# Optimization experiments

Measured on AMD Instinct MI355X. Metric: run time of the kernel, lower is better.

## Reference

```python
import jax, jax.numpy as jnp
from jax import lax
import numpy as np

T, B, D = 1024, 2, 1024
E, TOP_K, ED, HD, MAXP = 12, 4, 256, 64, 64
H = ED // HD  # num_heads = 4


def setup_inputs() -> dict:
    rng = jax.random.key(0)
    ks = jax.random.split(rng, 9)
    s = 0.02
    return {
        "query": jax.random.normal(ks[0], (T, B, D), jnp.float32),
        "key": jax.random.normal(ks[1], (T, B, D), jnp.float32),
        "value": jax.random.normal(ks[2], (T, B, D), jnp.float32),
        "w_gate": jax.random.normal(ks[3], (D, E), jnp.float32) * s,
        "w_map": jax.random.normal(ks[4], (E, D, ED), jnp.float32) * s,
        "w_reduce": jax.random.normal(ks[5], (E, ED, D), jnp.float32) * s,
        "wk": jax.random.normal(ks[6], (D, ED), jnp.float32) * s,
        "wv": jax.random.normal(ks[7], (D, ED), jnp.float32) * s,
        "rel_pos_emb": jax.random.normal(ks[8], (H, HD, 2 * MAXP + 1), jnp.float32) * s,
    }


def reference(query, key, value, w_gate, w_map, w_reduce, wk, wv, rel_pos_emb):
    t, b, d = query.shape
    n = t * b
    scaling = HD ** (-0.25)

    # ---- MoE map (q projection): softmax gating, top-k dispatch ----
    x = query.reshape(n, d)
    probs = jax.nn.softmax(x @ w_gate, axis=-1)          # [N,E]
    gates, idx = lax.top_k(probs, TOP_K)                 # [N,K]
    all_map = jnp.einsum('nd,edh->neh', x, w_map)        # [N,E,ED]
    q = jnp.take_along_axis(all_map, idx[:, :, None], axis=1)  # [N,K,ED]

    # ---- dense k/v projections ----
    q = (q * scaling).reshape(t, b, TOP_K, H, HD).transpose(1, 2, 3, 0, 4)  # [B,K,H,T,HD]
    k = (key.reshape(n, d) @ wk * scaling).reshape(t, b, H, HD).transpose(1, 2, 0, 3)  # [B,H,S,HD]
    v = (value.reshape(n, d) @ wv).reshape(t, b, H, HD).transpose(1, 2, 0, 3)          # [B,H,S,HD]

    # ---- attention scores ----
    aw = jnp.einsum('bkhie,bhje->bkhij', q, k)           # [B,K,H,T,S]

    # ---- relative position logits (einsum + gather) ----
    s_len = t
    pos = jnp.arange(s_len)
    grid = jnp.clip(pos[None, :] - pos[:, None], 1 - MAXP, MAXP - 1) + MAXP  # [T,S]
    rel = jnp.einsum('bkhid,hdp->bkhip', q, rel_pos_emb)  # [B,K,H,T,2*MAXP+1]
    rel_g = rel[:, :, :, jnp.arange(t)[:, None], grid]    # [B,K,H,T,S]

    aw = jax.nn.softmax(aw + rel_g, axis=-1)
    attn = jnp.einsum('bkhij,bhje->bkhie', aw, v)         # [B,K,H,T,HD]

    # ---- MoE reduce (combine with gates) ----
    a = attn.transpose(3, 0, 1, 2, 4).reshape(n, TOP_K, ED)  # [N,K,ED]
    one_hot = jax.nn.one_hot(idx, E, dtype=a.dtype)          # [N,K,E]
    z = jnp.einsum('nkh,nke,nk->neh', a, one_hot, gates)     # [N,E,ED]
    out = jnp.einsum('neh,ehd->nd', z, w_reduce)             # [N,D]
    return out.reshape(t, b, d)
```

## Files before the change

kernel.cpp:

```cpp
#include <hip/hip_runtime.h>

#define T_    1024
#define B_    2
#define D_    1024
#define E_    12
#define TOPK  4
#define ED_   256
#define HD_   64
#define H_    4
#define N_    (T_*B_)
#define NROW  (N_*TOPK)
#define PB3_MAX 76
#define KA_   256

typedef __bf16 bf16x8 __attribute__((ext_vector_type(8)));
typedef _Float16 f16x8 __attribute__((ext_vector_type(8)));
typedef float  f32x4  __attribute__((ext_vector_type(4)));

__device__ __forceinline__ float sc_() { return 0.35355339059327373f; }

__device__ __forceinline__ void async16(const void* g, void* l) {
    __builtin_amdgcn_global_load_lds((const __attribute__((address_space(1))) void*)g,
                                     (__attribute__((address_space(3))) void*)l, 16, 0, 0);
}

#define PREP_GRID 8324
__global__ void __launch_bounds__(256)
prep_kernel(const float* __restrict__ query, const float* __restrict__ key,
            const float* __restrict__ value, const float* __restrict__ wg,
            const float* __restrict__ wmap, const float* __restrict__ wred,
            const float* __restrict__ wk, const float* __restrict__ wv,
            const float* __restrict__ rpe,
            float* __restrict__ gates, int* __restrict__ idx, ushort* __restrict__ xb,
            ushort* __restrict__ keyb, ushort* __restrict__ valb,
            ushort* __restrict__ wmapT, ushort* __restrict__ wredf,
            ushort* __restrict__ wkT, ushort* __restrict__ wvT,
            ushort* __restrict__ rpeT, float* __restrict__ out) {
    __shared__ __align__(16) float lsbuf[12288];
    int bid = blockIdx.x, tid = threadIdx.x;

    if (bid < 512) {
        float (*lsw)[1024] = (float(*)[1024])lsbuf;
        for (int i = tid; i < 12288; i += 256) {
            int d = i / 12, e = i - d * 12;
            lsw[e][d] = wg[i];
        }
        __syncthreads();
        int w = tid >> 6, L = tid & 63;
        int n = bid * 4 + w;
        const float* xr = query + (size_t)n * D_;
        float acc[E_];
#pragma unroll
        for (int e = 0; e < E_; ++e) acc[e] = 0.f;
#pragma unroll
        for (int it = 0; it < 4; ++it) {
            float4 xv = *(const float4*)(xr + it * 256 + L * 4);
            union { __bf16 h[4]; uint2 u; } pk;
            pk.h[0] = (__bf16)xv.x; pk.h[1] = (__bf16)xv.y;
            pk.h[2] = (__bf16)xv.z; pk.h[3] = (__bf16)xv.w;
            *(uint2*)(xb + (size_t)n * D_ + it * 256 + L * 4) = pk.u;
#pragma unroll
            for (int e = 0; e < E_; ++e) {
                float4 wvv = *(const float4*)(&lsw[e][it * 256 + L * 4]);
                acc[e] += xv.x * wvv.x + xv.y * wvv.y + xv.z * wvv.z + xv.w * wvv.w;
            }
        }
#pragma unroll
        for (int e = 0; e < E_; ++e) {
            float v = acc[e];
            for (int o = 32; o > 0; o >>= 1) v += __shfl_down(v, o);
            acc[e] = v;
        }
        if (L == 0) {
            float mx = acc[0];
            for (int e = 1; e < E_; ++e) mx = fmaxf(mx, acc[e]);
            float s = 0.f, pr[E_];
            for (int e = 0; e < E_; ++e) { pr[e] = expf(acc[e] - mx); s += pr[e]; }
            float inv = 1.f / s;
            for (int e = 0; e < E_; ++e) pr[e] *= inv;
            for (int k = 0; k < TOPK; ++k) {
                int be = 0; float bv = -1.f;
                for (int e = 0; e < E_; ++e) if (pr[e] > bv) { bv = pr[e]; be = e; }
                gates[n * TOPK + k] = bv;
                idx[n * TOPK + k] = be;
                pr[be] = -1.f;
            }
        }
    } else if (bid < 1280) {
        float (*ls)[65] = (float(*)[65])lsbuf;
        int i = bid - 512;
        int e = i >> 6, rem = i & 63, et = rem >> 4, dt = rem & 15;
        int c = tid & 63, rg = tid >> 6;
        const float* src = wred + (size_t)e * (ED_ * D_) + (size_t)(et * 64) * D_ + dt * 64;
#pragma unroll
        for (int q = 0; q < 16; ++q) {
            int r = q * 4 + rg;
            ls[r][c] = src[(size_t)r * D_ + c];
        }
        __syncthreads();
        ushort* dst = wredf + (size_t)e * (D_ * KA_) + (size_t)(dt * 64) * KA_ + et * 64;
#pragma unroll
        for (int q = 0; q < 16; ++q) {
            int r = q * 4 + rg;
            union { _Float16 h; ushort u; } cv; cv.h = (_Float16)ls[c][r];
            dst[(size_t)r * KA_ + c] = cv.u;
        }
    } else if (bid < 5376) {
        int g = (bid - 1280) * 256 + tid;
        int which = g >> 19, t = g & ((1 << 19) - 1);
        const float* src = which ? value : key;
        ushort* dst = which ? valb : keyb;
        float4 v = *(const float4*)(src + (size_t)t * 4);
        union { __bf16 h[4]; uint2 u; } pk;
        pk.h[0] = (__bf16)v.x; pk.h[1] = (__bf16)v.y;
        pk.h[2] = (__bf16)v.z; pk.h[3] = (__bf16)v.w;
        *(uint2*)(dst + (size_t)t * 4) = pk.u;
    } else if (bid < 6144) {
        float (*ls)[65] = (float(*)[65])lsbuf;
        int i = bid - 5376;
        int e = i >> 6, rem = i & 63, dt = rem >> 2, et = rem & 3;
        int c = tid & 63, rg = tid >> 6;
        const float* src = wmap + (size_t)e * (D_ * ED_) + (size_t)(dt * 64) * ED_ + et * 64;
#pragma unroll
        for (int q = 0; q < 16; ++q) {
            int r = q * 4 + rg;
            ls[r][c] = src[(size_t)r * ED_ + c];
        }
        __syncthreads();
        ushort* dst = wmapT + ((size_t)e << 18) + (size_t)(et * 64) * 1024 + dt * 64;
#pragma unroll
        for (int q = 0; q < 16; ++q) {
            int r = q * 4 + rg;
            union { __bf16 h; ushort u; } cv; cv.h = (__bf16)ls[c][r];
            dst[(size_t)r * 1024 + c] = cv.u;
        }
    } else if (bid < 8192) {
        int t = (bid - 6144) * 256 + tid;
        *(float4*)(out + (size_t)t * 4) = make_float4(0.f, 0.f, 0.f, 0.f);
    } else if (bid < 8320) {
        float (*ls)[65] = (float(*)[65])lsbuf;
        int i = bid - 8192;
        int which = i >> 6, rem = i & 63, dt = rem >> 2, et = rem & 3;
        const float* w = which ? wv : wk;
        ushort* wT = which ? wvT : wkT;
        int c = tid & 63, rg = tid >> 6;
        const float* src = w + (size_t)(dt * 64) * ED_ + et * 64;
#pragma unroll
        for (int q = 0; q < 16; ++q) {
            int r = q * 4 + rg;
            ls[r][c] = src[(size_t)r * ED_ + c];
        }
        __syncthreads();
        ushort* dst = wT + (size_t)(et * 64) * 1024 + dt * 64;
#pragma unroll
        for (int q = 0; q < 16; ++q) {
            int r = q * 4 + rg;
            union { __bf16 h; ushort u; } cv; cv.h = (__bf16)ls[c][r];
            dst[(size_t)r * 1024 + c] = cv.u;
        }
    } else {
        int h = bid - 8320;
        int p = tid & 127, dq = tid >> 7;
#pragma unroll
        for (int d0 = 0; d0 < 64; d0 += 2) {
            int d = d0 + dq;
            union { __bf16 b; ushort u; } cv;
            cv.b = (__bf16)rpe[(size_t)(h * 64 + d) * 129 + p];
            rpeT[(size_t)(h * 128 + p) * 64 + d] = cv.u;
        }
    }
}

__global__ void __launch_bounds__(1024)
hss_kernel(const int* __restrict__ idx,
           int* __restrict__ rbe3, int* __restrict__ rbs3, int* __restrict__ rbc3,
           int* __restrict__ perm) {
    __shared__ int cnt[128][E_];
    __shared__ int pref[128][E_];
    __shared__ int offl[E_ + 1];
    __shared__ int counts[E_];
    int tid = threadIdx.x, w = tid >> 6, L = tid & 63;
    int mye[8];
#pragma unroll
    for (int g = 0; g < 8; ++g) {
        int c = w * 8 + g;
        int e = idx[c * 64 + L];
        mye[g] = e;
#pragma unroll
        for (int e0 = 0; e0 < E_; ++e0) {
            unsigned long long m = __ballot(e == e0);
            if (L == 0) cnt[c][e0] = (int)__popcll(m);
        }
    }
    __syncthreads();
    if (tid < E_) {
        int s = 0;
        for (int c = 0; c < 128; ++c) { pref[c][tid] = s; s += cnt[c][tid]; }
        counts[tid] = s;
    }
    __syncthreads();
    if (tid == 0) {
        int o = 0;
        for (int e = 0; e < E_; ++e) { offl[e] = o; o += counts[e]; }
        offl[E_] = o;
    }
    __syncthreads();
    if (tid < E_) {
        int pos = 0;
        for (int e = 0; e < tid; ++e) pos += (counts[e] + 127) >> 7;
        int c0 = counts[tid];
        for (int s = 0, k = 0; s < c0; s += 128, ++k) {
            rbe3[pos + k] = tid; rbs3[pos + k] = offl[tid] + s;
            int rem = c0 - s; rbc3[pos + k] = rem < 128 ? rem : 128;
        }
    }
    int tot = 0;
    for (int e = 0; e < E_; ++e) tot += (counts[e] + 127) >> 7;
    for (int i = tot + tid; i < PB3_MAX; i += 1024) {
        rbe3[i] = 0; rbs3[i] = 0; rbc3[i] = 0;
    }
#pragma unroll
    for (int g = 0; g < 8; ++g) {
        int c = w * 8 + g;
        int e = mye[g];
        int rank = 0;
#pragma unroll
        for (int e0 = 0; e0 < E_; ++e0) {
            unsigned long long m = __ballot(e == e0);
            if (e == e0) rank = (int)__popcll(m & ((1ULL << L) - 1ULL));
        }
        perm[offl[e] + pref[c][e] + rank] = c * 64 + L;
    }
}

__device__ __forceinline__ void mfma_k16_bf16(
    const ushort* const asrc[4], const ushort* bsrc,
    ushort As[2][128 * 64], ushort Bs[2][128 * 64],
    f32x4 acc[2][8], int w, int L) {
    auto stage = [&](int kt, int bf) {
#pragma unroll
        for (int q = 0; q < 4; ++q)
            async16(asrc[q] + kt * 64, &As[bf][(q * 32 + w * 8) * 64]);
#pragma unroll
        for (int q = 0; q < 4; ++q)
            async16(bsrc + (size_t)(q * 32) * 1024 + kt * 64, &Bs[bf][(q * 32 + w * 8) * 64]);
    };
    auto compute = [&](int bf) {
        const ushort* AB = As[bf] + w * 32 * 64;
        const ushort* BB = Bs[bf];
#pragma unroll
        for (int ks = 0; ks < 2; ++ks) {
            int phys = (((ks * 4 + (L >> 4)) ^ (L & 7))) * 8;
            bf16x8 a0 = *(const bf16x8*)(AB + (L & 15) * 64 + phys);
            bf16x8 a1 = *(const bf16x8*)(AB + (16 + (L & 15)) * 64 + phys);
#pragma unroll
            for (int nt = 0; nt < 8; ++nt) {
                bf16x8 bfr = *(const bf16x8*)(BB + (nt * 16 + (L & 15)) * 64 + phys);
                acc[0][nt] = __builtin_amdgcn_mfma_f32_16x16x32_bf16(a0, bfr, acc[0][nt], 0, 0, 0);
                acc[1][nt] = __builtin_amdgcn_mfma_f32_16x16x32_bf16(a1, bfr, acc[1][nt], 0, 0, 0);
            }
        }
    };
    stage(0, 0);
    for (int t = 0; t < 16; ++t) {
        __syncthreads();
        if (t < 15) stage(t + 1, (t + 1) & 1);
        compute(t & 1);
    }
}

__global__ void __launch_bounds__(256)
proj_mfma(const ushort* __restrict__ keyb, const ushort* __restrict__ valb,
          const ushort* __restrict__ wkT, const ushort* __restrict__ wvT,
          const ushort* __restrict__ xb, const ushort* __restrict__ wmapT,
          const int* __restrict__ perm,
          const int* __restrict__ rbe3, const int* __restrict__ rbs3,
          const int* __restrict__ rbc3,
          ushort* __restrict__ kpb, ushort* __restrict__ vpT,
          ushort* __restrict__ qpb) {
    __shared__ __align__(16) ushort As[2][128 * 64];
    __shared__ __align__(16) ushort Bs[2][128 * 64];
    __shared__ int rows3[128];
    int tid = threadIdx.x, w = tid >> 6, L = tid & 63;
    int swz = ((L & 7) ^ ((L >> 3) & 7)) * 8;

    f32x4 acc[2][8];
#pragma unroll
    for (int mt = 0; mt < 2; ++mt)
#pragma unroll
        for (int nt = 0; nt < 8; ++nt) acc[mt][nt] = (f32x4){0.f, 0.f, 0.f, 0.f};

    if (blockIdx.x < 64) {
        int which = blockIdx.x >> 5;
        int n0 = ((blockIdx.x >> 4) & 1) * 128;
        int mc = blockIdx.x & 15;
        int b = mc >> 3, t0 = (mc & 7) * 128;
        const ushort* xsrc = which ? valb : keyb;
        const ushort* wT = which ? wvT : wkT;
        const ushort* asrc[4];
#pragma unroll
        for (int q = 0; q < 4; ++q) {
            int rl = q * 32 + w * 8 + (L >> 3);
            int an = (((t0 + rl) << 1) | b);
            asrc[q] = xsrc + (size_t)an * 1024 + swz;
        }
        const ushort* bsrc = wT + (size_t)(n0 + w * 8 + (L >> 3)) * 1024 + swz;

        mfma_k16_bf16(asrc, bsrc, As, Bs, acc, w, L);

#pragma unroll
        for (int mt = 0; mt < 2; ++mt)
#pragma unroll
            for (int nt = 0; nt < 8; ++nt) {
                int ed = n0 + nt * 16 + (L & 15);
                int tb = t0 + w * 32 + mt * 16 + (L >> 4) * 4;
                if (which == 0) {
#pragma unroll
                    for (int r = 0; r < 4; ++r) {
                        union { __bf16 h; ushort u; } cv;
                        cv.h = (__bf16)(acc[mt][nt][r] * sc_());
                        kpb[((size_t)((b << 10) + tb + r)) * ED_ + ed] = cv.u;
                    }
                } else {
                    int h = ed >> 6, d = ed & 63;
                    union { __bf16 h4[4]; uint2 u; } pk;
#pragma unroll
                    for (int r = 0; r < 4; ++r) pk.h4[r] = (__bf16)acc[mt][nt][r];
                    *(uint2*)&vpT[((size_t)((b * 4 + h) * 64 + d)) * 1024 + tb] = pk.u;
                }
            }
    } else {
        int qid = blockIdx.x - 64;
        int blk = qid >> 1;
        int n0 = (qid & 1) * 128;
        int nr = rbc3[blk];
        if (nr == 0) return;
        int e = rbe3[blk], rs = rbs3[blk];
        if (tid < 128) rows3[tid] = (tid < nr) ? perm[rs + tid] : -1;
        __syncthreads();

        const ushort* asrc[4];
#pragma unroll
        for (int q = 0; q < 4; ++q) {
            int ar = rows3[q * 32 + w * 8 + (L >> 3)];
            asrc[q] = xb + (size_t)((ar < 0 ? 0 : ar) >> 2) * 1024 + swz;
        }
        const ushort* bsrc = wmapT + ((size_t)e << 18)
                           + (size_t)(n0 + w * 8 + (L >> 3)) * 1024 + swz;

        mfma_k16_bf16(asrc, bsrc, As, Bs, acc, w, L);

#pragma unroll
        for (int mt = 0; mt < 2; ++mt)
#pragma unroll
            for (int nt = 0; nt < 8; ++nt) {
                int n = n0 + nt * 16 + (L & 15);
#pragma unroll
                for (int r = 0; r < 4; ++r) {
                    int m = w * 32 + mt * 16 + (L >> 4) * 4 + r;
                    int rowg = rows3[m];
                    if (rowg >= 0) {
                        union { __bf16 h; ushort u; } cv;
                        cv.h = (__bf16)(acc[mt][nt][r] * sc_());
                        qpb[(size_t)rowg * ED_ + n] = cv.u;
                    }
                }
            }
    }
}

__global__ void __launch_bounds__(256)
rel_mfma(const ushort* __restrict__ qpb, const ushort* __restrict__ rpeT,
         ushort* __restrict__ relh) {
    int m0 = blockIdx.x * 128;
    int h  = blockIdx.y;
    int tid = threadIdx.x, w = tid >> 6, L = tid & 63;
    __shared__ __align__(16) ushort As[128 * 64];
    __shared__ __align__(16) ushort Bs[128 * 64];

    int swz = ((L & 7) ^ ((L >> 3) & 7)) * 8;
    const ushort* asrc = qpb + (size_t)(m0 + w * 8 + (L >> 3)) * ED_ + h * HD_ + swz;
    const ushort* bsrc = rpeT + (size_t)(h * 128 + w * 8 + (L >> 3)) * 64 + swz;
#pragma unroll
    for (int q = 0; q < 4; ++q) {
        async16(asrc + (size_t)(q * 32) * ED_, &As[(q * 32 + w * 8) * 64]);
        async16(bsrc + (size_t)(q * 32) * 64,  &Bs[(q * 32 + w * 8) * 64]);
    }
    __syncthreads();

    f32x4 acc[2][8];
#pragma unroll
    for (int mt = 0; mt < 2; ++mt)
#pragma unroll
        for (int nt = 0; nt < 8; ++nt) acc[mt][nt] = (f32x4){0.f, 0.f, 0.f, 0.f};

    const ushort* AB = As + w * 32 * 64;
#pragma unroll
    for (int ks = 0; ks < 2; ++ks) {
        int phys = (((ks * 4 + (L >> 4)) ^ (L & 7))) * 8;
        bf16x8 a0 = *(const bf16x8*)(AB + (L & 15) * 64 + phys);
        bf16x8 a1 = *(const bf16x8*)(AB + (16 + (L & 15)) * 64 + phys);
#pragma unroll
        for (int nt = 0; nt < 8; ++nt) {
            bf16x8 b = *(const bf16x8*)(Bs + (nt * 16 + (L & 15)) * 64 + phys);
            acc[0][nt] = __builtin_amdgcn_mfma_f32_16x16x32_bf16(a0, b, acc[0][nt], 0, 0, 0);
            acc[1][nt] = __builtin_amdgcn_mfma_f32_16x16x32_bf16(a1, b, acc[1][nt], 0, 0, 0);
        }
    }

#pragma unroll
    for (int mt = 0; mt < 2; ++mt)
#pragma unroll
        for (int nt = 0; nt < 8; ++nt) {
            int p = nt * 16 + (L & 15);
#pragma unroll
            for (int r = 0; r < 4; ++r) {
                int qrow = m0 + w * 32 + mt * 16 + (L >> 4) * 4 + r;
                union { _Float16 h16; ushort u; } cv;
                cv.h16 = (_Float16)acc[mt][nt][r];
                relh[((size_t)qrow * 4 + h) * 128 + p] = cv.u;
            }
        }
}

__global__ void __launch_bounds__(256)
attn_kernel(const ushort* __restrict__ qpb, const ushort* __restrict__ kpb,
            const ushort* __restrict__ vpT, const ushort* __restrict__ relh,
            const float* __restrict__ gates, ushort* __restrict__ az) {
    __shared__ __align__(16) ushort Ks[2][64 * 64];
    __shared__ __align__(16) ushort Vs[2][64 * 64];
    __shared__ __align__(16) ushort Ps[4][16 * 64];

    const int tid = threadIdx.x;
    const int w = tid >> 6, L = tid & 63;
    const int bkh = blockIdx.x & 31, it = blockIdx.x >> 5;
    const int h = bkh & 3, kk = (bkh >> 2) & 3, bb = bkh >> 4;
    const int i0w = it * 64 + w * 16;
    const int iL = i0w + (L & 15);
    const int row = ((iL * 2 + bb) << 2) | kk;

    const ushort* qrow = qpb + row * ED_ + h * HD_;
    bf16x8 qf0 = *(const bf16x8*)(qrow + (L >> 4) * 8);
    bf16x8 qf1 = *(const bf16x8*)(qrow + 32 + (L >> 4) * 8);

    const ushort* relrow = relh + ((size_t)row * 4 + h) * 128;
    float rel_lo = (float)*(const _Float16*)(relrow + 1);
    float rel_hi = (float)*(const _Float16*)(relrow + 127);
    float gate = gates[row];

    f32x4 O[4];
#pragma unroll
    for (int mf = 0; mf < 4; ++mf) O[mf] = (f32x4){0.f, 0.f, 0.f, 0.f};
    float l_acc = 0.f;

    const ushort* ksrc = kpb + (size_t)(bb << 10) * ED_ + h * HD_;
    const ushort* vsrc = vpT + (size_t)((bb * 4 + h) * 64) * 1024;

    auto stage = [&](int t, int bf) {
        int j0 = t * 64;
#pragma unroll
        for (int q = 0; q < 2; ++q) {
            int r = L >> 3;
            int c = (L & 7) ^ r;
            const ushort* src = ksrc + (size_t)(j0 + w * 16 + q * 8 + r) * ED_ + c * 8;
            async16(src, &Ks[bf][(w * 16 + q * 8) * 64]);
        }
#pragma unroll
        for (int q = 0; q < 2; ++q) {
            int r = L >> 3;
            int d = w * 16 + q * 8 + r;
            int c = (L & 7) ^ (d & 7);
            const ushort* src = vsrc + (size_t)d * 1024 + j0 + c * 8;
            async16(src, &Vs[bf][(w * 16 + q * 8) * 64]);
        }
    };

    auto compute = [&](int bf, int j0) {
        const ushort* KB = Ks[bf];
        const ushort* VB = Vs[bf];
        ushort* PW = Ps[w];
#pragma unroll
        for (int jf = 0; jf < 4; ++jf) {
            int jrow = jf * 16 + (L & 15);
            bf16x8 a0 = *(const bf16x8*)(KB + jrow * 64 + (((L >> 4)) ^ (L & 7)) * 8);
            bf16x8 a1 = *(const bf16x8*)(KB + jrow * 64 + ((4 + (L >> 4)) ^ (L & 7)) * 8);
            f32x4 s = (f32x4){0.f, 0.f, 0.f, 0.f};
            s = __builtin_amdgcn_mfma_f32_16x16x32_bf16(a0, qf0, s, 0, 0, 0);
            s = __builtin_amdgcn_mfma_f32_16x16x32_bf16(a1, qf1, s, 0, 0, 0);
            int jlo = j0 + jf * 16;
            int jbase = jlo + (L >> 4) * 4;
            float pv[4];
            if (jlo >= i0w + 78) {
#pragma unroll
                for (int r = 0; r < 4; ++r) pv[r] = __expf(s[r] + rel_hi);
            } else if (jlo <= i0w - 78) {
#pragma unroll
                for (int r = 0; r < 4; ++r) pv[r] = __expf(s[r] + rel_lo);
            } else {
#pragma unroll
                for (int r = 0; r < 4; ++r) {
                    int dj = jbase + r - iL;
                    dj = dj < -63 ? -63 : (dj > 63 ? 63 : dj);
                    pv[r] = __expf(s[r] + (float)*(const _Float16*)(relrow + dj + 64));
                }
            }
            l_acc += (pv[0] + pv[1]) + (pv[2] + pv[3]);
            union { __bf16 h4[4]; uint2 u; } pk;
#pragma unroll
            for (int r = 0; r < 4; ++r) pk.h4[r] = (__bf16)pv[r];
            int iloc = L & 15;
            int chunk = jf * 2 + ((L >> 4) >> 1);
            int phys = chunk ^ (iloc & 7);
            *(uint2*)(PW + iloc * 64 + phys * 8 + ((L >> 4) & 1) * 4) = pk.u;
        }
#pragma unroll
        for (int ks = 0; ks < 2; ++ks) {
            int c = ks * 4 + (L >> 4);
            int phys = c ^ (L & 7);
            bf16x8 pf = *(const bf16x8*)(PW + (L & 15) * 64 + phys * 8);
#pragma unroll
            for (int mf = 0; mf < 4; ++mf) {
                bf16x8 vf = *(const bf16x8*)(VB + (mf * 16 + (L & 15)) * 64 + phys * 8);
                O[mf] = __builtin_amdgcn_mfma_f32_16x16x32_bf16(vf, pf, O[mf], 0, 0, 0);
            }
        }
    };

    stage(0, 0);
    for (int t = 0; t < 16; ++t) {
        __syncthreads();
        if (t < 15) stage(t + 1, (t + 1) & 1);
        compute(t & 1, t * 64);
    }

    l_acc += __shfl_xor(l_acc, 16);
    l_acc += __shfl_xor(l_acc, 32);
    float inv = gate / l_acc;
    ushort* azrow = az + (size_t)row * KA_ + h * HD_;
#pragma unroll
    for (int mf = 0; mf < 4; ++mf) {
        union { _Float16 h4[4]; uint2 u; } pk;
#pragma unroll
        for (int r = 0; r < 4; ++r) pk.h4[r] = (_Float16)(O[mf][r] * inv);
        int off = mf * 16 + (L >> 4) * 4;
        *(uint2*)(azrow + off) = pk.u;
    }
}

__global__ void __launch_bounds__(256)
reduce_mfma(const ushort* __restrict__ az, const ushort* __restrict__ wredf,
            const int* __restrict__ perm,
            const int* __restrict__ rbe3, const int* __restrict__ rbs3,
            const int* __restrict__ rbc3, float* __restrict__ out) {
    int blk = blockIdx.x;
    int nr = rbc3[blk];
    if (nr == 0) return;
    int e = rbe3[blk], rs = rbs3[blk];
    int n0 = blockIdx.y * 128;
    int tid = threadIdx.x, w = tid >> 6, L = tid & 63;
    __shared__ __align__(16) ushort As[2][128 * 64];
    __shared__ __align__(16) ushort Bs[2][128 * 64];
    __shared__ int rows3[128];
    if (tid < 128) rows3[tid] = (tid < nr) ? perm[rs + tid] : -1;
    __syncthreads();

    int swz = ((L & 7) ^ ((L >> 3) & 7)) * 8;
    const ushort* asrc[4];
#pragma unroll
    for (int q = 0; q < 4; ++q) {
        int ar = rows3[q * 32 + w * 8 + (L >> 3)];
        asrc[q] = az + (size_t)(ar < 0 ? 0 : ar) * KA_ + swz;
    }
    const ushort* bsrc = wredf + (size_t)e * (D_ * KA_)
                       + (size_t)(n0 + w * 8 + (L >> 3)) * KA_ + swz;

    f32x4 acc[2][8];
#pragma unroll
    for (int mt = 0; mt < 2; ++mt)
#pragma unroll
        for (int nt = 0; nt < 8; ++nt) acc[mt][nt] = (f32x4){0.f, 0.f, 0.f, 0.f};

    auto stage = [&](int kt, int bf) {
#pragma unroll
        for (int q = 0; q < 4; ++q)
            async16(asrc[q] + kt * 64, &As[bf][(q * 32 + w * 8) * 64]);
#pragma unroll
        for (int q = 0; q < 4; ++q)
            async16(bsrc + (size_t)(q * 32) * KA_ + kt * 64, &Bs[bf][(q * 32 + w * 8) * 64]);
    };
    auto compute = [&](int bf) {
        const ushort* AB = As[bf] + w * 32 * 64;
        const ushort* BB = Bs[bf];
#pragma unroll
        for (int ks = 0; ks < 2; ++ks) {
            int phys = (((ks * 4 + (L >> 4)) ^ (L & 7))) * 8;
            f16x8 a0 = *(const f16x8*)(AB + (L & 15) * 64 + phys);
            f16x8 a1 = *(const f16x8*)(AB + (16 + (L & 15)) * 64 + phys);
#pragma unroll
            for (int nt = 0; nt < 8; ++nt) {
                f16x8 b = *(const f16x8*)(BB + (nt * 16 + (L & 15)) * 64 + phys);
                acc[0][nt] = __builtin_amdgcn_mfma_f32_16x16x32_f16(a0, b, acc[0][nt], 0, 0, 0);
                acc[1][nt] = __builtin_amdgcn_mfma_f32_16x16x32_f16(a1, b, acc[1][nt], 0, 0, 0);
            }
        }
    };

    stage(0, 0);
    for (int t = 0; t < 4; ++t) {
        __syncthreads();
        if (t < 3) stage(t + 1, (t + 1) & 1);
        compute(t & 1);
    }

#pragma unroll
    for (int mt = 0; mt < 2; ++mt)
#pragma unroll
        for (int nt = 0; nt < 8; ++nt) {
            int n = n0 + nt * 16 + (L & 15);
#pragma unroll
            for (int r = 0; r < 4; ++r) {
                int m = w * 32 + mt * 16 + (L >> 4) * 4 + r;
                int rowg = rows3[m];
                if (rowg >= 0)
                    unsafeAtomicAdd(out + (size_t)(rowg >> 2) * D_ + n, acc[mt][nt][r]);
            }
        }
}

extern "C" void kernel_launch(void* const* d_in, const int* in_sizes, int n_in,
                              void* d_out, int out_size, void* d_ws, size_t ws_size,
                              hipStream_t stream) {
    const float* query = (const float*)d_in[0];
    const float* key   = (const float*)d_in[1];
    const float* value = (const float*)d_in[2];
    const float* wg    = (const float*)d_in[3];
    const float* wmap  = (const float*)d_in[4];
    const float* wred  = (const float*)d_in[5];
    const float* wk    = (const float*)d_in[6];
    const float* wv    = (const float*)d_in[7];
    const float* rpe   = (const float*)d_in[8];
    float* out = (float*)d_out;

    char* ws = (char*)d_ws;
    float*  gates = (float*)(ws + 0);
    int*    idx   = (int*)(ws + (32 << 10));
    char*   misc  = ws + (64 << 10);
    int*    rbe3   = (int*)(misc + 12288);
    int*    rbs3   = (int*)(misc + 12800);
    int*    rbc3   = (int*)(misc + 13312);
    int*    perm  = (int*)(ws + (96 << 10));
    char*   base_ = ws + (128 << 10);
    ushort* rpeT  = (ushort*)(base_);
    ushort* qpb   = (ushort*)(base_ + (8u  << 20));
    ushort* kpb   = (ushort*)(base_ + (12u << 20));
    ushort* vpT   = (ushort*)(base_ + (13u << 20));
    ushort* xb    = (ushort*)(base_ + (14u << 20));
    ushort* wmapT = (ushort*)(base_ + (18u << 20));
    ushort* keyb  = (ushort*)(base_ + (24u << 20));
    ushort* valb  = (ushort*)(base_ + (28u << 20));
    ushort* wkT   = (ushort*)(base_ + (32u << 20));
    ushort* wvT   = (ushort*)(base_ + (32u << 20) + (512u << 10));
    ushort* az    = (ushort*)(base_ + (48u << 20));
    ushort* wredf = (ushort*)(base_ + (61u << 20));
    ushort* relh  = (ushort*)(base_ + (80u << 20));

    prep_kernel<<<PREP_GRID, 256, 0, stream>>>(query, key, value, wg, wmap, wred,
        wk, wv, rpe, gates, idx, xb, keyb, valb, wmapT, wredf, wkT, wvT, rpeT, out);
    hss_kernel<<<1, 1024, 0, stream>>>(idx, rbe3, rbs3, rbc3, perm);
    proj_mfma<<<64 + 2 * PB3_MAX, 256, 0, stream>>>(keyb, valb, wkT, wvT, xb, wmapT,
        perm, rbe3, rbs3, rbc3, kpb, vpT, qpb);
    rel_mfma<<<dim3(64, 4), 256, 0, stream>>>(qpb, rpeT, relh);
    attn_kernel<<<512, 256, 0, stream>>>(qpb, kpb, vpT, relh, gates, az);
    reduce_mfma<<<dim3(PB3_MAX, 8), 256, 0, stream>>>(az, wredf, perm, rbe3, rbs3, rbc3, out);
}
```

Before: 220.6 us.

## Fuse relative-position logits computation into attention kernel prologue

Removes the separate rel_mfma launch and its fp16 global relh buffer. Each attention block now loads the 128 rpeT rows for its head into the K staging buffers, computes q·rel via MFMA for its 64 query rows, and keeps the fp32 results in a new ~33KB LDS array. This saves one kernel launch and the global write and read of the rel table, and keeps the logits in fp32. The cost is extra LDS per block, which may lower occupancy, plus a serial prologue with two barriers before the main loop.

Measured after the change: 213.2 us. 1.03x faster.

```diff
diff --git a/kernel.cpp b/kernel.cpp
--- a/kernel.cpp
+++ b/kernel.cpp
@@ -370,66 +370,13 @@
 }
 
 __global__ void __launch_bounds__(256)
-rel_mfma(const ushort* __restrict__ qpb, const ushort* __restrict__ rpeT,
-         ushort* __restrict__ relh) {
-    int m0 = blockIdx.x * 128;
-    int h  = blockIdx.y;
-    int tid = threadIdx.x, w = tid >> 6, L = tid & 63;
-    __shared__ __align__(16) ushort As[128 * 64];
-    __shared__ __align__(16) ushort Bs[128 * 64];
-
-    int swz = ((L & 7) ^ ((L >> 3) & 7)) * 8;
-    const ushort* asrc = qpb + (size_t)(m0 + w * 8 + (L >> 3)) * ED_ + h * HD_ + swz;
-    const ushort* bsrc = rpeT + (size_t)(h * 128 + w * 8 + (L >> 3)) * 64 + swz;
-#pragma unroll
-    for (int q = 0; q < 4; ++q) {
-        async16(asrc + (size_t)(q * 32) * ED_, &As[(q * 32 + w * 8) * 64]);
-        async16(bsrc + (size_t)(q * 32) * 64,  &Bs[(q * 32 + w * 8) * 64]);
-    }
-    __syncthreads();
-
-    f32x4 acc[2][8];
-#pragma unroll
-    for (int mt = 0; mt < 2; ++mt)
-#pragma unroll
-        for (int nt = 0; nt < 8; ++nt) acc[mt][nt] = (f32x4){0.f, 0.f, 0.f, 0.f};
-
-    const ushort* AB = As + w * 32 * 64;
-#pragma unroll
-    for (int ks = 0; ks < 2; ++ks) {
-        int phys = (((ks * 4 + (L >> 4)) ^ (L & 7))) * 8;
-        bf16x8 a0 = *(const bf16x8*)(AB + (L & 15) * 64 + phys);
-        bf16x8 a1 = *(const bf16x8*)(AB + (16 + (L & 15)) * 64 + phys);
-#pragma unroll
-        for (int nt = 0; nt < 8; ++nt) {
-            bf16x8 b = *(const bf16x8*)(Bs + (nt * 16 + (L & 15)) * 64 + phys);
-            acc[0][nt] = __builtin_amdgcn_mfma_f32_16x16x32_bf16(a0, b, acc[0][nt], 0, 0, 0);
-            acc[1][nt] = __builtin_amdgcn_mfma_f32_16x16x32_bf16(a1, b, acc[1][nt], 0, 0, 0);
-        }
-    }
-
-#pragma unroll
-    for (int mt = 0; mt < 2; ++mt)
-#pragma unroll
-        for (int nt = 0; nt < 8; ++nt) {
-            int p = nt * 16 + (L & 15);
-#pragma unroll
-            for (int r = 0; r < 4; ++r) {
-                int qrow = m0 + w * 32 + mt * 16 + (L >> 4) * 4 + r;
-                union { _Float16 h16; ushort u; } cv;
-                cv.h16 = (_Float16)acc[mt][nt][r];
-                relh[((size_t)qrow * 4 + h) * 128 + p] = cv.u;
-            }
-        }
-}
-
-__global__ void __launch_bounds__(256)
 attn_kernel(const ushort* __restrict__ qpb, const ushort* __restrict__ kpb,
-            const ushort* __restrict__ vpT, const ushort* __restrict__ relh,
+            const ushort* __restrict__ vpT, const ushort* __restrict__ rpeT,
             const float* __restrict__ gates, ushort* __restrict__ az) {
     __shared__ __align__(16) ushort Ks[2][64 * 64];
     __shared__ __align__(16) ushort Vs[2][64 * 64];
     __shared__ __align__(16) ushort Ps[4][16 * 64];
+    __shared__ __align__(16) float ls_rel[64 * 132];
 
     const int tid = threadIdx.x;
     const int w = tid >> 6, L = tid & 63;
@@ -443,10 +390,35 @@
     bf16x8 qf0 = *(const bf16x8*)(qrow + (L >> 4) * 8);
     bf16x8 qf1 = *(const bf16x8*)(qrow + 32 + (L >> 4) * 8);
 
-    const ushort* relrow = relh + ((size_t)row * 4 + h) * 128;
-    float rel_lo = (float)*(const _Float16*)(relrow + 1);
-    float rel_hi = (float)*(const _Float16*)(relrow + 127);
     float gate = gates[row];
+
+    {
+        int r = L >> 3;
+        int c = (L & 7) ^ r;
+        const ushort* rsrc = rpeT + (size_t)(h * 128) * 64 + c * 8;
+#pragma unroll
+        for (int q = 0; q < 2; ++q) {
+            int p0 = w * 16 + q * 8 + r;
+            async16(rsrc + (size_t)p0 * 64, &Ks[0][(w * 16 + q * 8) * 64]);
+            async16(rsrc + (size_t)(64 + p0) * 64, &Ks[1][(w * 16 + q * 8) * 64]);
+        }
+    }
+    __syncthreads();
+#pragma unroll
+    for (int pt = 0; pt < 8; ++pt) {
+        const ushort* RB = Ks[pt >> 2];
+        int prow = (pt & 3) * 16 + (L & 15);
+        bf16x8 a0 = *(const bf16x8*)(RB + prow * 64 + (((L >> 4)) ^ (L & 7)) * 8);
+        bf16x8 a1 = *(const bf16x8*)(RB + prow * 64 + ((4 + (L >> 4)) ^ (L & 7)) * 8);
+        f32x4 s = (f32x4){0.f, 0.f, 0.f, 0.f};
+        s = __builtin_amdgcn_mfma_f32_16x16x32_bf16(a0, qf0, s, 0, 0, 0);
+        s = __builtin_amdgcn_mfma_f32_16x16x32_bf16(a1, qf1, s, 0, 0, 0);
+        *(f32x4*)&ls_rel[(w * 16 + (L & 15)) * 132 + pt * 16 + (L >> 4) * 4] = s;
+    }
+    __syncthreads();
+
+    const float* relrow = &ls_rel[(w * 16 + (L & 15)) * 132];
+    float rel_lo = relrow[1], rel_hi = relrow[127];
 
     f32x4 O[4];
 #pragma unroll
@@ -501,7 +473,7 @@
                 for (int r = 0; r < 4; ++r) {
                     int dj = jbase + r - iL;
                     dj = dj < -63 ? -63 : (dj > 63 ? 63 : dj);
-                    pv[r] = __expf(s[r] + (float)*(const _Float16*)(relrow + dj + 64));
+                    pv[r] = __expf(s[r] + relrow[dj + 64]);
                 }
             }
             l_acc += (pv[0] + pv[1]) + (pv[2] + pv[3]);
@@ -662,14 +634,12 @@
     ushort* wvT   = (ushort*)(base_ + (32u << 20) + (512u << 10));
     ushort* az    = (ushort*)(base_ + (48u << 20));
     ushort* wredf = (ushort*)(base_ + (61u << 20));
-    ushort* relh  = (ushort*)(base_ + (80u << 20));
 
     prep_kernel<<<PREP_GRID, 256, 0, stream>>>(query, key, value, wg, wmap, wred,
         wk, wv, rpe, gates, idx, xb, keyb, valb, wmapT, wredf, wkT, wvT, rpeT, out);
     hss_kernel<<<1, 1024, 0, stream>>>(idx, rbe3, rbs3, rbc3, perm);
     proj_mfma<<<64 + 2 * PB3_MAX, 256, 0, stream>>>(keyb, valb, wkT, wvT, xb, wmapT,
         perm, rbe3, rbs3, rbc3, kpb, vpT, qpb);
-    rel_mfma<<<dim3(64, 4), 256, 0, stream>>>(qpb, rpeT, relh);
-    attn_kernel<<<512, 256, 0, stream>>>(qpb, kpb, vpT, relh, gates, az);
+    attn_kernel<<<512, 256, 0, stream>>>(qpb, kpb, vpT, rpeT, gates, az);
     reduce_mfma<<<dim3(PB3_MAX, 8), 256, 0, stream>>>(az, wredf, perm, rbe3, rbs3, rbc3, out);
 }
```
